# Optimization experiments

Measured on AMD Instinct MI355X. Metric: run time of the kernel, lower is better.

## Reference

```python
import jax, jax.numpy as jnp
import numpy as np

K = 16  # number of neighbors (module init arg)

def setup_inputs() -> dict:
    key = jax.random.key(0)
    M, D, N = 65536, 16, 64
    x = jax.random.normal(key, (M, D), dtype=jnp.float32)
    # equal-length segments: each point set has M // N points
    segs = jnp.full((N,), M // N, dtype=jnp.int64)
    return {"x": x, "segs": segs}

def reference(x, segs):
    # Segmented kNN graph. Segments are equal-length (static shapes for jit),
    # so the per-segment pairwise distance + top-k becomes a batched op.
    B = segs.shape[0]
    M, D = x.shape
    L = M // B  # points per segment
    pts = x.reshape(B, L, D)
    # squared euclidean distances within each segment: (B, L, L)
    sq = jnp.sum(pts * pts, axis=-1)
    d2 = sq[:, :, None] + sq[:, None, :] - 2.0 * jnp.einsum('bld,bmd->blm', pts, pts)
    # k smallest distances per point (includes self, as in DGL's knn_graph)
    _, idx = jax.lax.top_k(-d2, K)  # idx: (B, L, K), local indices within segment
    offsets = (jnp.arange(B, dtype=idx.dtype) * L)[:, None, None]
    src = (idx + offsets).reshape(-1)                      # neighbor -> global node id
    dst = (jnp.arange(L, dtype=idx.dtype)[None, :, None] + offsets)  # (B, L, 1)
    dst = jnp.broadcast_to(dst, (B, L, K)).reshape(-1)
    # edges point from k-nearest neighbors (predecessors) to each node
    return src, dst
```

## Files before the change

kernel.cpp:

```cpp
#include <hip/hip_runtime.h>
#include <stdint.h>


#define L_SEG 1024
#define M_PTS 65536

typedef __fp16 fp16x2 __attribute__((ext_vector_type(2)));
typedef __fp16 fp16x4 __attribute__((ext_vector_type(4)));
typedef float  f32x4  __attribute__((ext_vector_type(4)));

__device__ __forceinline__ uint32_t umn(uint32_t a, uint32_t b) { return a < b ? a : b; }
__device__ __forceinline__ uint32_t umx(uint32_t a, uint32_t b) { return a > b ? a : b; }

#define CE(arr, i, p) { uint32_t lo = umn(arr[i], arr[p]); uint32_t hi = umx(arr[i], arr[p]); arr[i] = lo; arr[p] = hi; }

__device__ __forceinline__ void clean16(uint32_t* A) {
    #pragma unroll
    for (int j = 8; j > 0; j >>= 1) {
        #pragma unroll
        for (int i = 0; i < 16; ++i) {
            int p = i ^ j;
            if (p > i) CE(A, i, p);
        }
    }
}

__device__ __forceinline__ void sort16(uint32_t* B) {
    #pragma unroll
    for (int p = 1; p < 16; p <<= 1) {
        #pragma unroll
        for (int k = p; k >= 1; k >>= 1) {
            #pragma unroll
            for (int j = (k & (p - 1)); j + k < 16; j += 2 * k) {
                #pragma unroll
                for (int i = 0; i <= ((k - 1 < 15 - j - k) ? k - 1 : 15 - j - k); ++i) {
                    if ((i + j) / (2 * p) == (i + j + k) / (2 * p)) CE(B, i + j, i + j + k);
                }
            }
        }
    }
}

__device__ __forceinline__ void keep16(uint32_t* A, const uint32_t* S) {
    #pragma unroll
    for (int i = 0; i < 16; ++i) A[i] = umn(A[i], S[15 - i]);
    clean16(A);
}

__device__ __forceinline__ void mergeg(uint32_t* A) {
    #pragma unroll
    for (int m = 16; m <= 32; m <<= 1) {
        uint32_t P[16];
        #pragma unroll
        for (int i = 0; i < 16; ++i) P[i] = (uint32_t)__shfl_xor((int)A[15 - i], m, 64);
        #pragma unroll
        for (int i = 0; i < 16; ++i) A[i] = umn(A[i], P[i]);
        clean16(A);
    }
}

__device__ __forceinline__ uint32_t sel4(const uint32_t* A, int g, int v) {
    uint32_t t01 = (g & 1) ? A[4 + v]  : A[v];
    uint32_t t23 = (g & 1) ? A[12 + v] : A[8 + v];
    return (g & 2) ? t23 : t01;
}

__global__ __launch_bounds__(256, 4) void knn_v9_kernel(const float* __restrict__ x,
                                                        int* __restrict__ out) {
    __shared__ __attribute__((aligned(16))) __fp16 sc[L_SEG * 16];
    __shared__ __attribute__((aligned(16))) float  ssq[L_SEG];
    __shared__ __attribute__((aligned(16))) __fp16 sq16[64 * 16];

    const int tid = threadIdx.x;
    const int b   = blockIdx.x;
    const int seg = (b & 7) * 8 + (b >> 7);
    const int qp  = (b >> 3) & 15;
    const float* xseg = x + (size_t)seg * (L_SEG * 16);
    const f32x4* gx4  = (const f32x4*)xseg;

    {
        fp16x4* scv = (fp16x4*)sc;
        #pragma unroll
        for (int i = 0; i < 16; ++i) {
            f32x4 v = gx4[tid + 256 * i];
            union { fp16x2 h2[2]; fp16x4 h4; } u;
            u.h2[0] = __builtin_amdgcn_cvt_pkrtz(-2.0f * v[0], -2.0f * v[1]);
            u.h2[1] = __builtin_amdgcn_cvt_pkrtz(-2.0f * v[2], -2.0f * v[3]);
            scv[tid + 256 * i] = u.h4;
        }
    }
    {
        const int c0 = tid << 2;
        #pragma unroll
        for (int c = 0; c < 4; ++c) {
            float s = 128.0f;
            #pragma unroll
            for (int d = 0; d < 4; ++d) {
                f32x4 v = gx4[(c0 + c) * 4 + d];
                s = __builtin_fmaf(v[0], v[0], s);
                s = __builtin_fmaf(v[1], v[1], s);
                s = __builtin_fmaf(v[2], v[2], s);
                s = __builtin_fmaf(v[3], v[3], s);
            }
            ssq[c0 + c] = s;
        }
    }
    if (tid < 64) {
        const f32x4* qg = gx4 + (size_t)(qp * 64 + tid) * 4;
        fp16x4* dst = (fp16x4*)(sq16 + (size_t)tid * 16);
        #pragma unroll
        for (int d = 0; d < 4; ++d) {
            f32x4 v = qg[d];
            union { fp16x2 h2[2]; fp16x4 h4; } u;
            u.h2[0] = __builtin_amdgcn_cvt_pkrtz(v[0], v[1]);
            u.h2[1] = __builtin_amdgcn_cvt_pkrtz(v[2], v[3]);
            dst[d] = u.h4;
        }
    }
    __syncthreads();

    const int lane = tid & 63;
    const int w    = tid >> 6;
    const int g    = lane >> 4;
    const int col  = lane & 15;
    const int qloc = qp * 64 + w * 16 + col;

    const fp16x4 bfrag = *(const fp16x4*)(sq16 + (size_t)(w * 16 + col) * 16 + g * 4);

    uint32_t A[16];
    #pragma unroll
    for (int i = 0; i < 16; ++i) A[i] = 0xFFFFFFFFu;

    const __fp16* ap  = sc + (size_t)col * 16 + g * 4;
    const float*  sqp = ssq + g * 4;
    const uint32_t vg4 = (uint32_t)(g << 2);

    #pragma unroll 2
    for (int it = 0; it < 4; ++it) {
        uint32_t P[16];
        #pragma unroll
        for (int t = 0; t < 16; ++t) {
            const int cb = it * 256 + t * 16;
            fp16x4 af = *(const fp16x4*)(ap + (size_t)cb * 16);
            f32x4  sq = *(const f32x4*)(sqp + cb);
            f32x4 acc = __builtin_amdgcn_mfma_f32_16x16x16f16(af, bfrag, sq, 0, 0, 0);
            const uint32_t ib = (uint32_t)cb + vg4;
            uint32_t k0 = (__float_as_uint(acc[0]) & 0xFFFFFC00u) | ib;
            uint32_t k1 = (__float_as_uint(acc[1]) & 0xFFFFFC00u) | (ib + 1u);
            uint32_t k2 = (__float_as_uint(acc[2]) & 0xFFFFFC00u) | (ib + 2u);
            uint32_t k3 = (__float_as_uint(acc[3]) & 0xFFFFFC00u) | (ib + 3u);
            P[t] = umn(umn(k0, k1), umn(k2, k3));
        }
        sort16(P);
        keep16(A, P);
    }

    mergeg(A);

    union H8 { f32x4 v[2]; fp16x2 h2[8]; };
    H8 qq;
    {
        const f32x4* qf = (const f32x4*)(sq16 + (size_t)(w * 16 + col) * 16);
        qq.v[0] = qf[0]; qq.v[1] = qf[1];
    }
    uint32_t R[16];
    #pragma unroll
    for (int v = 0; v < 4; ++v) {
        const uint32_t win = sel4(A, g, v);
        const uint32_t wi  = win & 1023u;
        const uint32_t qb  = wi & ~3u;
        const uint32_t wo  = wi & 3u;
        #pragma unroll
        for (int k = 0; k < 3; ++k) {
            const uint32_t o    = (uint32_t)k + (((uint32_t)k >= wo) ? 1u : 0u);
            const uint32_t pidx = qb + o;
            H8 cc;
            const f32x4* cf = (const f32x4*)(sc + (size_t)pidx * 16);
            cc.v[0] = cf[0]; cc.v[1] = cf[1];
            float s = 0.0f;
            #pragma unroll
            for (int j = 0; j < 8; ++j) {
#if __has_builtin(__builtin_amdgcn_fdot2)
                s = __builtin_amdgcn_fdot2(cc.h2[j], qq.h2[j], s, false);
#else
                s = __builtin_fmaf((float)cc.h2[j][0], (float)qq.h2[j][0], s);
                s = __builtin_fmaf((float)cc.h2[j][1], (float)qq.h2[j][1], s);
#endif
            }
            const float val = s + ssq[pidx];
            R[v * 3 + k] = (__float_as_uint(val) & 0xFFFFFC00u) | pidx;
        }
    }
    #pragma unroll
    for (int i = 12; i < 16; ++i) R[i] = 0xFFFFFFFFu;
    sort16(R);
    mergeg(R);
    keep16(A, R);

    const int base = seg * L_SEG;
    const int q    = base + qloc;
    int4 sv;
    sv.x = base + (int)(sel4(A, g, 0) & 1023u);
    sv.y = base + (int)(sel4(A, g, 1) & 1023u);
    sv.z = base + (int)(sel4(A, g, 2) & 1023u);
    sv.w = base + (int)(sel4(A, g, 3) & 1023u);
    ((int4*)out)[(size_t)q * 4 + g] = sv;
    ((int4*)out)[(size_t)M_PTS * 4 + (size_t)q * 4 + g] = make_int4(q, q, q, q);
}

extern "C" void kernel_launch(void* const* d_in, const int* in_sizes, int n_in,
                              void* d_out, int out_size, void* d_ws, size_t ws_size,
                              hipStream_t stream) {
    const float* x = (const float*)d_in[0];
    int* out = (int*)d_out;
    (void)d_ws; (void)ws_size;
    knn_v9_kernel<<<dim3(1024), dim3(256), 0, stream>>>(x, out);
}
```

Before: 87.75 us.

## Use 1024-thread blocks per quarter segment and re-rank whole 4-point groups

Each block now has 1024 threads and handles 256 queries of one segment, so every segment is staged into LDS 4 times instead of 16. Squared norms come from a shuffle reduction during staging, and query fragments are taken from the scaled LDS copy instead of a separate query buffer. The first pass keeps the top-16 4-point groups using the group minimum, and the refine pass rescores all 4 members of each group with fdot2. The final top-16 is then drawn only from those rescored points. Fewer, larger blocks and the changed candidate selection may alter occupancy and approximation accuracy.

```diff
diff --git a/kernel.cpp b/kernel.cpp
--- a/kernel.cpp
+++ b/kernel.cpp
@@ -65,56 +65,34 @@
     return (g & 2) ? t23 : t01;
 }
 
-__global__ __launch_bounds__(256, 4) void knn_v9_kernel(const float* __restrict__ x,
-                                                        int* __restrict__ out) {
+__global__ __launch_bounds__(1024, 4) void knn_v10_kernel(const float* __restrict__ x,
+                                                          int* __restrict__ out) {
     __shared__ __attribute__((aligned(16))) __fp16 sc[L_SEG * 16];
     __shared__ __attribute__((aligned(16))) float  ssq[L_SEG];
-    __shared__ __attribute__((aligned(16))) __fp16 sq16[64 * 16];
-
-    const int tid = threadIdx.x;
-    const int b   = blockIdx.x;
-    const int seg = (b & 7) * 8 + (b >> 7);
-    const int qp  = (b >> 3) & 15;
+
+    const int tid  = threadIdx.x;
+    const int b    = blockIdx.x;
+    const int seg  = b >> 2;
+    const int qgrp = (b & 3) << 8;
     const float* xseg = x + (size_t)seg * (L_SEG * 16);
     const f32x4* gx4  = (const f32x4*)xseg;
 
     {
         fp16x4* scv = (fp16x4*)sc;
         #pragma unroll
-        for (int i = 0; i < 16; ++i) {
-            f32x4 v = gx4[tid + 256 * i];
+        for (int i = 0; i < 4; ++i) {
+            f32x4 v = gx4[tid + 1024 * i];
             union { fp16x2 h2[2]; fp16x4 h4; } u;
             u.h2[0] = __builtin_amdgcn_cvt_pkrtz(-2.0f * v[0], -2.0f * v[1]);
             u.h2[1] = __builtin_amdgcn_cvt_pkrtz(-2.0f * v[2], -2.0f * v[3]);
-            scv[tid + 256 * i] = u.h4;
-        }
-    }
-    {
-        const int c0 = tid << 2;
-        #pragma unroll
-        for (int c = 0; c < 4; ++c) {
-            float s = 128.0f;
-            #pragma unroll
-            for (int d = 0; d < 4; ++d) {
-                f32x4 v = gx4[(c0 + c) * 4 + d];
-                s = __builtin_fmaf(v[0], v[0], s);
-                s = __builtin_fmaf(v[1], v[1], s);
-                s = __builtin_fmaf(v[2], v[2], s);
-                s = __builtin_fmaf(v[3], v[3], s);
-            }
-            ssq[c0 + c] = s;
-        }
-    }
-    if (tid < 64) {
-        const f32x4* qg = gx4 + (size_t)(qp * 64 + tid) * 4;
-        fp16x4* dst = (fp16x4*)(sq16 + (size_t)tid * 16);
-        #pragma unroll
-        for (int d = 0; d < 4; ++d) {
-            f32x4 v = qg[d];
-            union { fp16x2 h2[2]; fp16x4 h4; } u;
-            u.h2[0] = __builtin_amdgcn_cvt_pkrtz(v[0], v[1]);
-            u.h2[1] = __builtin_amdgcn_cvt_pkrtz(v[2], v[3]);
-            dst[d] = u.h4;
+            scv[tid + 1024 * i] = u.h4;
+            float p = v[0] * v[0];
+            p = __builtin_fmaf(v[1], v[1], p);
+            p = __builtin_fmaf(v[2], v[2], p);
+            p = __builtin_fmaf(v[3], v[3], p);
+            p += __shfl_xor(p, 1, 64);
+            p += __shfl_xor(p, 2, 64);
+            if ((tid & 3) == 0) ssq[(tid >> 2) + 256 * i] = p + 128.0f;
         }
     }
     __syncthreads();
@@ -123,20 +101,36 @@
     const int w    = tid >> 6;
     const int g    = lane >> 4;
     const int col  = lane & 15;
-    const int qloc = qp * 64 + w * 16 + col;
-
-    const fp16x4 bfrag = *(const fp16x4*)(sq16 + (size_t)(w * 16 + col) * 16 + g * 4);
-
-    uint32_t A[16];
-    #pragma unroll
-    for (int i = 0; i < 16; ++i) A[i] = 0xFFFFFFFFu;
+    const int qrow = qgrp + w * 16 + col;
+
+    const fp16x4 mh = {(__fp16)-0.5f, (__fp16)-0.5f, (__fp16)-0.5f, (__fp16)-0.5f};
+    fp16x4 bfrag;
+    {
+        fp16x4 raw = *(const fp16x4*)(sc + (size_t)qrow * 16 + g * 4);
+        bfrag = raw * mh;
+    }
 
     const __fp16* ap  = sc + (size_t)col * 16 + g * 4;
     const float*  sqp = ssq + g * 4;
-    const uint32_t vg4 = (uint32_t)(g << 2);
-
-    #pragma unroll 2
-    for (int it = 0; it < 4; ++it) {
+
+    uint32_t A[16];
+    {
+        uint32_t P[16];
+        #pragma unroll
+        for (int t = 0; t < 16; ++t) {
+            const int cb = t * 16;
+            fp16x4 af = *(const fp16x4*)(ap + (size_t)cb * 16);
+            f32x4  sq = *(const f32x4*)(sqp + cb);
+            f32x4 acc = __builtin_amdgcn_mfma_f32_16x16x16f16(af, bfrag, sq, 0, 0, 0);
+            float m = fminf(fminf(fminf(acc[0], acc[1]), acc[2]), acc[3]);
+            P[t] = (__float_as_uint(m) & 0xFFFFFF00u) | (uint32_t)(t * 4) | (uint32_t)g;
+        }
+        sort16(P);
+        #pragma unroll
+        for (int i = 0; i < 16; ++i) A[i] = P[i];
+    }
+    #pragma unroll
+    for (int it = 1; it < 4; ++it) {
         uint32_t P[16];
         #pragma unroll
         for (int t = 0; t < 16; ++t) {
@@ -144,12 +138,8 @@
             fp16x4 af = *(const fp16x4*)(ap + (size_t)cb * 16);
             f32x4  sq = *(const f32x4*)(sqp + cb);
             f32x4 acc = __builtin_amdgcn_mfma_f32_16x16x16f16(af, bfrag, sq, 0, 0, 0);
-            const uint32_t ib = (uint32_t)cb + vg4;
-            uint32_t k0 = (__float_as_uint(acc[0]) & 0xFFFFFC00u) | ib;
-            uint32_t k1 = (__float_as_uint(acc[1]) & 0xFFFFFC00u) | (ib + 1u);
-            uint32_t k2 = (__float_as_uint(acc[2]) & 0xFFFFFC00u) | (ib + 2u);
-            uint32_t k3 = (__float_as_uint(acc[3]) & 0xFFFFFC00u) | (ib + 3u);
-            P[t] = umn(umn(k0, k1), umn(k2, k3));
+            float m = fminf(fminf(fminf(acc[0], acc[1]), acc[2]), acc[3]);
+            P[t] = (__float_as_uint(m) & 0xFFFFFF00u) | (uint32_t)(it * 64 + t * 4) | (uint32_t)g;
         }
         sort16(P);
         keep16(A, P);
@@ -157,27 +147,26 @@
 
     mergeg(A);
 
-    union H8 { f32x4 v[2]; fp16x2 h2[8]; };
+    union H8 { f32x4 v[2]; fp16x4 h4[2]; fp16x2 h2[8]; };
     H8 qq;
     {
-        const f32x4* qf = (const f32x4*)(sq16 + (size_t)(w * 16 + col) * 16);
+        const f32x4* qf = (const f32x4*)(sc + (size_t)qrow * 16);
         qq.v[0] = qf[0]; qq.v[1] = qf[1];
+        qq.h4[0] = qq.h4[0] * mh;
+        qq.h4[1] = qq.h4[1] * mh;
     }
     uint32_t R[16];
     #pragma unroll
     for (int v = 0; v < 4; ++v) {
-        const uint32_t win = sel4(A, g, v);
-        const uint32_t wi  = win & 1023u;
-        const uint32_t qb  = wi & ~3u;
-        const uint32_t wo  = wi & 3u;
-        #pragma unroll
-        for (int k = 0; k < 3; ++k) {
-            const uint32_t o    = (uint32_t)k + (((uint32_t)k >= wo) ? 1u : 0u);
-            const uint32_t pidx = qb + o;
+        const uint32_t qid   = sel4(A, g, v) & 255u;
+        const uint32_t pbase = qid << 2;
+        #pragma unroll
+        for (int m = 0; m < 4; ++m) {
+            const uint32_t pidx = pbase + (uint32_t)m;
             H8 cc;
             const f32x4* cf = (const f32x4*)(sc + (size_t)pidx * 16);
             cc.v[0] = cf[0]; cc.v[1] = cf[1];
-            float s = 0.0f;
+            float s = ssq[pidx];
             #pragma unroll
             for (int j = 0; j < 8; ++j) {
 #if __has_builtin(__builtin_amdgcn_fdot2)
@@ -187,23 +176,19 @@
                 s = __builtin_fmaf((float)cc.h2[j][1], (float)qq.h2[j][1], s);
 #endif
             }
-            const float val = s + ssq[pidx];
-            R[v * 3 + k] = (__float_as_uint(val) & 0xFFFFFC00u) | pidx;
-        }
-    }
-    #pragma unroll
-    for (int i = 12; i < 16; ++i) R[i] = 0xFFFFFFFFu;
+            R[v * 4 + m] = (__float_as_uint(s) & 0xFFFFFC00u) | pidx;
+        }
+    }
     sort16(R);
     mergeg(R);
-    keep16(A, R);
 
     const int base = seg * L_SEG;
-    const int q    = base + qloc;
+    const int q    = base + qrow;
     int4 sv;
-    sv.x = base + (int)(sel4(A, g, 0) & 1023u);
-    sv.y = base + (int)(sel4(A, g, 1) & 1023u);
-    sv.z = base + (int)(sel4(A, g, 2) & 1023u);
-    sv.w = base + (int)(sel4(A, g, 3) & 1023u);
+    sv.x = base + (int)(sel4(R, g, 0) & 1023u);
+    sv.y = base + (int)(sel4(R, g, 1) & 1023u);
+    sv.z = base + (int)(sel4(R, g, 2) & 1023u);
+    sv.w = base + (int)(sel4(R, g, 3) & 1023u);
     ((int4*)out)[(size_t)q * 4 + g] = sv;
     ((int4*)out)[(size_t)M_PTS * 4 + (size_t)q * 4 + g] = make_int4(q, q, q, q);
 }
@@ -214,5 +199,5 @@
     const float* x = (const float*)d_in[0];
     int* out = (int*)d_out;
     (void)d_ws; (void)ws_size;
-    knn_v9_kernel<<<dim3(1024), dim3(256), 0, stream>>>(x, out);
-}
+    knn_v10_kernel<<<dim3(256), dim3(1024), 0, stream>>>(x, out);
+}
```

New measurement: 84.26 us. 1.04x faster.
